# Kernel tuning notes

Hardware: AMD Instinct MI355X
Metric: run time of the kernel (lower is better)

## Reference

```python
import jax, jax.numpy as jnp
import numpy as np

N_HEAD = 12
ROPE_BASE = 10000.0


def rotate_half(x):
    h = x.shape[-1] // 2
    x1, x2 = x[..., :h], x[..., h:]
    return jnp.concatenate((-x2, x1), axis=-1)


def rope_cos_sin(T, head_dim, dtype):
    inv_freq = 1.0 / (ROPE_BASE ** (jnp.arange(0, head_dim, 2, dtype=jnp.float32) / head_dim))
    t = jnp.arange(T, dtype=jnp.float32)
    freqs = jnp.einsum('i,j->ij', t, inv_freq)          # [T, head_dim/2]
    emb = jnp.concatenate((freqs, freqs), axis=-1)       # [T, head_dim]
    return jnp.cos(emb).astype(dtype), jnp.sin(emb).astype(dtype)


def setup_inputs() -> dict:
    key = jax.random.key(0)
    ks = jax.random.split(key, 5)
    B, T, C = 1, 4096, 768
    return {
        'x': jax.random.normal(ks[0], (B, T, C), dtype=jnp.float32),
        'w_attn': jax.random.normal(ks[1], (C, 3 * C), dtype=jnp.float32) * (1.0 / np.sqrt(C)),
        'b_attn': jax.random.normal(ks[2], (3 * C,), dtype=jnp.float32) * 0.02,
        'w_proj': jax.random.normal(ks[3], (C, C), dtype=jnp.float32) * (1.0 / np.sqrt(C)),
        'b_proj': jax.random.normal(ks[4], (C,), dtype=jnp.float32) * 0.02,
    }


def reference(x, w_attn, b_attn, w_proj, b_proj):
    B, T, C = x.shape
    H = N_HEAD
    hd = C // H

    qkv = x @ w_attn + b_attn                            # [B, T, 3C]
    q, k, v = jnp.split(qkv, 3, axis=-1)
    q = q.reshape(B, T, H, hd)
    k = k.reshape(B, T, H, hd)
    v = v.reshape(B, T, H, hd)

    cos, sin = rope_cos_sin(T, hd, x.dtype)              # [T, hd]
    cos = cos[None, :, None, :]
    sin = sin[None, :, None, :]
    q = q * cos + rotate_half(q) * sin
    k = k * cos + rotate_half(k) * sin

    # [B, H, T, hd]
    q = q.transpose(0, 2, 1, 3)
    k = k.transpose(0, 2, 1, 3)
    v = v.transpose(0, 2, 1, 3)

    att = jnp.einsum('bhtd,bhsd->bhts', q, k) * (1.0 / np.sqrt(hd))
    causal_mask = jnp.triu(jnp.ones((T, T), dtype=bool), k=1)
    att = jnp.where(causal_mask, -jnp.inf, att)
    att = jax.nn.softmax(att, axis=-1)

    y = jnp.einsum('bhts,bhsd->bhtd', att, v)            # [B, H, T, hd]
    y = y.transpose(0, 2, 1, 3).reshape(B, T, C)
    return y @ w_proj + b_proj
```

## Files before the change

kernel.cpp:

```cpp
#include <hip/hip_runtime.h>
#include <hip/hip_bf16.h>
#include <math.h>

using bf16 = __hip_bfloat16;
typedef __bf16 bf16x8_t __attribute__((ext_vector_type(8)));
typedef float f32x4_t __attribute__((ext_vector_type(4)));

static __device__ __forceinline__ f32x4_t mfma16(bf16x8_t a, bf16x8_t b, f32x4_t c) {
    return __builtin_amdgcn_mfma_f32_16x16x32_bf16(a, b, c, 0, 0, 0);
}

#if __has_builtin(__builtin_amdgcn_exp2f)
#define EXP2F __builtin_amdgcn_exp2f
#else
#define EXP2F exp2f
#endif

static __device__ __forceinline__ void sincos_rev(float rev, float* s, float* c) {
    float f = rev - floorf(rev);
#if __has_builtin(__builtin_amdgcn_sinf) && __has_builtin(__builtin_amdgcn_cosf)
    *s = __builtin_amdgcn_sinf(f);
    *c = __builtin_amdgcn_cosf(f);
#else
    float th = f * 6.2831853071795864f;
    *s = __sinf(th); *c = __cosf(th);
#endif
}

static __device__ __forceinline__ void async16(bf16* lds, const bf16* g) {
    __builtin_amdgcn_global_load_lds(
        (const __attribute__((address_space(1))) unsigned int*)g,
        (__attribute__((address_space(3))) unsigned int*)lds, 16, 0, 0);
}

static __device__ __forceinline__ int detect_bf16(const unsigned short* u16) {
    const int lane = threadIdx.x & 63;
    int sane = 0;
#pragma unroll
    for (int j = 0; j < 4; ++j) {
        const unsigned short u = u16[2 * (lane * 4 + j)];
        const int e = (u >> 7) & 0xFF;
        if (u == 0 || (e >= 100 && e <= 150)) sane++;
    }
#pragma unroll
    for (int off = 1; off <= 32; off <<= 1) sane += __shfl_xor(sane, off);
    return (sane * 2 >= 256) ? 1 : 0;
}

static __device__ __forceinline__ float bias_at(const void* b, int i, int isbf) {
    return isbf ? __bfloat162float(((const bf16*)b)[i]) : ((const float*)b)[i];
}

static __device__ __forceinline__ void transpose_tile(
    const void* in, bf16* out, int in_ld, int out_ld, int bx, int by,
    int isbf, bf16 (*tile)[72]) {
    const int c0 = bx * 64, r0 = by * 64;
    const int tid = threadIdx.x;
    for (int c = tid; c < 512; c += 256) {
        const int r = c >> 3, co = (c & 7) << 3;
        if (isbf) {
            *reinterpret_cast<float4*>(&tile[r][co]) =
                *reinterpret_cast<const float4*>((const bf16*)in + (size_t)(r0 + r) * in_ld + c0 + co);
        } else {
            const float* f = (const float*)in + (size_t)(r0 + r) * in_ld + c0 + co;
            const float4 a = *reinterpret_cast<const float4*>(f);
            const float4 b = *reinterpret_cast<const float4*>(f + 4);
            tile[r][co + 0] = __float2bfloat16(a.x); tile[r][co + 1] = __float2bfloat16(a.y);
            tile[r][co + 2] = __float2bfloat16(a.z); tile[r][co + 3] = __float2bfloat16(a.w);
            tile[r][co + 4] = __float2bfloat16(b.x); tile[r][co + 5] = __float2bfloat16(b.y);
            tile[r][co + 6] = __float2bfloat16(b.z); tile[r][co + 7] = __float2bfloat16(b.w);
        }
    }
    __syncthreads();
    for (int c = tid; c < 512; c += 256) {
        const int r = c >> 3, co = (c & 7) << 3;
        union { float4 v; bf16 e[8]; } u;
#pragma unroll
        for (int j = 0; j < 8; ++j) u.e[j] = tile[co + j][r];
        *reinterpret_cast<float4*>(out + (size_t)(c0 + r) * out_ld + r0 + co) = u.v;
    }
}

__global__ __launch_bounds__(256) void prep_kernel(
    const void* __restrict__ x, const void* __restrict__ w_attn,
    const void* __restrict__ w_proj, bf16* __restrict__ xb,
    bf16* __restrict__ wAT, bf16* __restrict__ wPT) {
    __shared__ bf16 tile[64][72];
    const int isbf = detect_bf16((const unsigned short*)x);
    const int b = blockIdx.x;
    if (b < 432) {
        transpose_tile(w_attn, wAT, 2304, 768, b % 36, b / 36, isbf, tile);
    } else if (b < 576) {
        const int bb = b - 432;
        transpose_tile(w_proj, wPT, 768, 768, bb % 12, bb / 12, isbf, tile);
    } else {
        const int i = ((b - 576) * 256 + threadIdx.x) * 8;
        if (isbf) {
            *reinterpret_cast<float4*>(xb + i) =
                *reinterpret_cast<const float4*>((const bf16*)x + i);
        } else {
            const float* f = (const float*)x + i;
            const float4 a = *reinterpret_cast<const float4*>(f);
            const float4 c = *reinterpret_cast<const float4*>(f + 4);
            union { float4 v; bf16 e[8]; } u;
            u.e[0] = __float2bfloat16(a.x); u.e[1] = __float2bfloat16(a.y);
            u.e[2] = __float2bfloat16(a.z); u.e[3] = __float2bfloat16(a.w);
            u.e[4] = __float2bfloat16(c.x); u.e[5] = __float2bfloat16(c.y);
            u.e[6] = __float2bfloat16(c.z); u.e[7] = __float2bfloat16(c.w);
            *reinterpret_cast<float4*>(xb + i) = u.v;
        }
    }
}

template <int MI>
__global__ __launch_bounds__(256, MI == 4 ? 3 : 4) void gemm_kernel(
    const bf16* __restrict__ A, const bf16* __restrict__ Bt,
    const void* __restrict__ bias, bf16* __restrict__ C,
    bf16* __restrict__ VtOut, const unsigned short* __restrict__ xdet,
    int N, int K, int mode, int flexout) {
    constexpr int MT = MI * 32;
    __shared__ bf16 smem[(MT + 128) * 64];
    bf16* sa = smem;
    bf16* sb = smem + MT * 64;
    const int tid = threadIdx.x, lane = tid & 63, w = tid >> 6;
    const int wm = w >> 1, wn = w & 1, quad = lane >> 4, l16 = lane & 15;
    const int m0 = blockIdx.y * MT, n0 = blockIdx.x * 128;
    const int strow = lane >> 3, stslot = lane & 7;

    const bf16* ag[MI]; const bf16* bgp[4];
#pragma unroll
    for (int i = 0; i < MI; ++i) {
        const int r = (w * MI + i) * 8 + strow;
        ag[i] = A + (size_t)(m0 + r) * K + (stslot ^ (r & 7)) * 8;
    }
#pragma unroll
    for (int i = 0; i < 4; ++i) {
        const int r = (w * 4 + i) * 8 + strow;
        bgp[i] = Bt + (size_t)(n0 + r) * K + (stslot ^ (r & 7)) * 8;
    }

    f32x4_t acc[MI][4];
#pragma unroll
    for (int i = 0; i < MI; ++i)
#pragma unroll
        for (int j = 0; j < 4; ++j) acc[i][j] = (f32x4_t){0.f, 0.f, 0.f, 0.f};

    for (int k0 = 0; k0 < K; k0 += 64) {
        __syncthreads();
#pragma unroll
        for (int i = 0; i < MI; ++i) async16(&sa[(w * MI + i) * 512], ag[i] + k0);
#pragma unroll
        for (int i = 0; i < 4; ++i)  async16(&sb[(w * 4 + i) * 512], bgp[i] + k0);
        __asm__ __volatile__("s_waitcnt vmcnt(0)" ::: "memory");
        __syncthreads();

#pragma unroll
        for (int kk = 0; kk < 2; ++kk) {
            bf16x8_t af[MI], bf_[4];
#pragma unroll
            for (int mi = 0; mi < MI; ++mi) {
                const int r = wm * (MI * 16) + mi * 16 + l16;
                af[mi] = *reinterpret_cast<const bf16x8_t*>(
                    &sa[r * 64 + (((kk * 4 + quad) ^ (r & 7)) << 3)]);
            }
#pragma unroll
            for (int ni = 0; ni < 4; ++ni) {
                const int r = wn * 64 + ni * 16 + l16;
                bf_[ni] = *reinterpret_cast<const bf16x8_t*>(
                    &sb[r * 64 + (((kk * 4 + quad) ^ (r & 7)) << 3)]);
            }
#pragma unroll
            for (int mi = 0; mi < MI; ++mi)
#pragma unroll
                for (int ni = 0; ni < 4; ++ni)
                    acc[mi][ni] = mfma16(af[mi], bf_[ni], acc[mi][ni]);
        }
    }

    const int isbf = detect_bf16(xdet);
    const int f32out = flexout && !isbf;
    const int colbase = n0 + wn * 64;
    const int rowbase = m0 + wm * (MI * 16);
    if (mode == 1 && colbase < 1536) {
        const bool isq = colbase < 768;
        const float QS = 0.18033688011112042f;
#pragma unroll
        for (int ni = 0; ni < 2; ++ni) {
            const int d = ni * 16 + l16;
            const int col_lo = colbase + d, col_hi = col_lo + 32;
            const float blo = bias_at(bias, col_lo, isbf);
            const float bhi = bias_at(bias, col_hi, isbf);
            const float invf_rev = powf(10000.0f, -(float)d * (1.0f / 32.0f)) * 0.15915494309189535f;
#pragma unroll
            for (int mi = 0; mi < MI; ++mi) {
#pragma unroll
                for (int rg = 0; rg < 4; ++rg) {
                    const int t = rowbase + mi * 16 + quad * 4 + rg;
                    float sv, cv;
                    sincos_rev((float)t * invf_rev, &sv, &cv);
                    const float lo = acc[mi][ni][rg] + blo;
                    const float hi = acc[mi][ni + 2][rg] + bhi;
                    float nlo = lo * cv - hi * sv;
                    float nhi = hi * cv + lo * sv;
                    if (isq) { nlo *= QS; nhi *= QS; }
                    C[(size_t)t * N + col_lo] = __float2bfloat16(nlo);
                    C[(size_t)t * N + col_hi] = __float2bfloat16(nhi);
                }
            }
        }
    } else if (mode == 1) {
        if constexpr (MI == 4) {
            __syncthreads();
            bf16* T = smem + w * 2304;
            const int vcb = colbase - 1536;
#pragma unroll
            for (int pass = 0; pass < 2; ++pass) {
                if (pass) __asm__ __volatile__("s_waitcnt lgkmcnt(0)" ::: "memory");
#pragma unroll
                for (int nl = 0; nl < 2; ++nl) {
                    const int ni = pass * 2 + nl;
                    const float b = bias_at(bias, colbase + ni * 16 + l16, isbf);
                    const int dh = nl * 16 + l16;
#pragma unroll
                    for (int rg = 0; rg < 4; ++rg) {
                        union { int2 v; bf16 e[4]; } pk;
#pragma unroll
                        for (int mi = 0; mi < 4; ++mi)
                            pk.e[mi] = __float2bfloat16(acc[mi][ni][rg] + b);
                        *reinterpret_cast<int2*>(&T[dh * 72 + quad * 16 + rg * 4]) = pk.v;
                    }
                }
                __asm__ __volatile__("s_waitcnt lgkmcnt(0)" ::: "memory");
#pragma unroll
                for (int s = 0; s < 4; ++s) {
                    const int dh = s * 8 + (lane >> 3);
                    const int pj = lane & 7;
                    const float4 vv = *reinterpret_cast<const float4*>(&T[dh * 72 + pj * 8]);
                    *reinterpret_cast<float4*>(
                        &VtOut[(size_t)(vcb + pass * 32 + dh) * 4096 + rowbase + pj * 8]) = vv;
                }
            }
        }
    } else {
#pragma unroll
        for (int ni = 0; ni < 4; ++ni) {
            const int col = colbase + ni * 16 + l16;
            const float b = bias_at(bias, col, isbf);
#pragma unroll
            for (int mi = 0; mi < MI; ++mi) {
#pragma unroll
                for (int rg = 0; rg < 4; ++rg) {
                    const int t = rowbase + mi * 16 + quad * 4 + rg;
                    const float v = acc[mi][ni][rg] + b;
                    if (f32out) ((float*)C)[(size_t)t * N + col] = v;
                    else        C[(size_t)t * N + col] = __float2bfloat16(v);
                }
            }
        }
    }
}

__global__ __launch_bounds__(128, 3) void attn_kernel(
    const bf16* __restrict__ qkv, const bf16* __restrict__ Vt,
    bf16* __restrict__ ybuf, bf16* __restrict__ po, float* __restrict__ pl) {
    const int h = blockIdx.y;
    const int bx = blockIdx.x;
    int qt, c, nc;
    if (bx < 16)      { qt = bx;                 c = 0;             nc = 1; }
    else if (bx < 48) { qt = 16 + (bx - 16) / 2; c = (bx - 16) % 2; nc = 2; }
    else if (bx < 96) { qt = 32 + (bx - 48) / 3; c = (bx - 48) % 3; nc = 3; }
    else              { qt = 48 + (bx - 96) / 4; c = (bx - 96) % 4; nc = 4; }
    const int kt0 = c * 16;
    const int kt1 = min(kt0 + 16, qt + 1);

    const int tid = threadIdx.x, lane = tid & 63, w = tid >> 6;
    const int quad = lane >> 4, l16 = lane & 15, sw = l16 & 7;

    __shared__ bf16 Kt[2][4096];
    __shared__ bf16 Pt[2][2][16][72];

    const int strow = lane >> 3, stslot = lane & 7;
    const bf16* kg[4];
#pragma unroll
    for (int i = 0; i < 4; ++i) {
        const int key = (w * 4 + i) * 8 + strow;
        kg[i] = qkv + (size_t)key * 2304 + 768 + h * 64 + (stslot ^ (key & 7)) * 8;
    }
    const bf16* vbase = Vt + (size_t)(h * 64) * 4096;

    const int qbase = qt * 64 + w * 32;
    bf16x8_t qf[2][2];
#pragma unroll
    for (int f = 0; f < 2; ++f)
#pragma unroll
        for (int kc = 0; kc < 2; ++kc)
            qf[f][kc] = *reinterpret_cast<const bf16x8_t*>(
                qkv + (size_t)(qbase + f * 16 + l16) * 2304 + h * 64 + kc * 32 + quad * 8);

    f32x4_t o[2][4];
#pragma unroll
    for (int f = 0; f < 2; ++f)
#pragma unroll
        for (int dt = 0; dt < 4; ++dt) o[f][dt] = (f32x4_t){0.f, 0.f, 0.f, 0.f};
    float l_i[2][4] = {{0.f, 0.f, 0.f, 0.f}, {0.f, 0.f, 0.f, 0.f}};

#pragma unroll
    for (int i = 0; i < 4; ++i)
        async16(&Kt[0][(w * 4 + i) * 512], kg[i] + (size_t)kt0 * 64 * 2304);
    __asm__ __volatile__("s_waitcnt vmcnt(0)" ::: "memory");
    __syncthreads();

    for (int kt = kt0; kt < kt1; ++kt) {
        const int b = (kt - kt0) & 1;
        if (kt + 1 < kt1) {
#pragma unroll
            for (int i = 0; i < 4; ++i)
                async16(&Kt[b ^ 1][(w * 4 + i) * 512], kg[i] + (size_t)(kt + 1) * 64 * 2304);
        }
        bf16x8_t vf[2][4];
#pragma unroll
        for (int kc = 0; kc < 2; ++kc)
#pragma unroll
            for (int dt = 0; dt < 4; ++dt)
                vf[kc][dt] = *reinterpret_cast<const bf16x8_t*>(
                    vbase + (size_t)(dt * 16 + l16) * 4096 + kt * 64 + kc * 32 + quad * 8);

        bf16x8_t kf[2][4];
#pragma unroll
        for (int kc = 0; kc < 2; ++kc)
#pragma unroll
            for (int ct = 0; ct < 4; ++ct)
                kf[kc][ct] = *reinterpret_cast<const bf16x8_t*>(
                    &Kt[b][((ct * 16 + l16) << 6) + (((kc * 4 + quad) ^ sw) << 3)]);

        f32x4_t s[2][4];
#pragma unroll
        for (int f = 0; f < 2; ++f)
#pragma unroll
            for (int ct = 0; ct < 4; ++ct) {
                s[f][ct] = mfma16(qf[f][0], kf[0][ct], (f32x4_t){0.f, 0.f, 0.f, 0.f});
                s[f][ct] = mfma16(qf[f][1], kf[1][ct], s[f][ct]);
            }

        if (kt == qt) {
#pragma unroll
            for (int f = 0; f < 2; ++f) {
                const int rowb = qbase + f * 16 + quad * 4;
#pragma unroll
                for (int ct = 0; ct < 4; ++ct) {
                    const int key = kt * 64 + ct * 16 + l16;
#pragma unroll
                    for (int rg = 0; rg < 4; ++rg)
                        if (key > rowb + rg) s[f][ct][rg] = -INFINITY;
                }
            }
        }

#pragma unroll
        for (int f = 0; f < 2; ++f)
#pragma unroll
            for (int ct = 0; ct < 4; ++ct)
#pragma unroll
                for (int rg = 0; rg < 4; ++rg) {
                    const float p = EXP2F(s[f][ct][rg]);
                    s[f][ct][rg] = p;
                    l_i[f][rg] += p;
                }

#pragma unroll
        for (int f = 0; f < 2; ++f)
#pragma unroll
            for (int rg = 0; rg < 4; ++rg) {
                union { int2 v; __hip_bfloat162 h2[2]; } pk;
                pk.h2[0] = __float22bfloat162_rn(float2{s[f][0][rg], s[f][1][rg]});
                pk.h2[1] = __float22bfloat162_rn(float2{s[f][2][rg], s[f][3][rg]});
                *reinterpret_cast<int2*>(&Pt[w][f][quad * 4 + rg][l16 * 4]) = pk.v;
            }
        __asm__ __volatile__("s_waitcnt lgkmcnt(0)" ::: "memory");

#pragma unroll
        for (int f = 0; f < 2; ++f)
#pragma unroll
            for (int kc = 0; kc < 2; ++kc) {
                const bf16x8_t pf =
                    *reinterpret_cast<const bf16x8_t*>(&Pt[w][f][l16][kc * 32 + quad * 8]);
#pragma unroll
                for (int dt = 0; dt < 4; ++dt)
                    o[f][dt] = mfma16(pf, vf[kc][dt], o[f][dt]);
            }

        __asm__ __volatile__("s_waitcnt vmcnt(0)" ::: "memory");
        __syncthreads();
    }

#pragma unroll
    for (int off = 1; off <= 8; off <<= 1)
#pragma unroll
        for (int f = 0; f < 2; ++f)
#pragma unroll
            for (int rg = 0; rg < 4; ++rg) l_i[f][rg] += __shfl_xor(l_i[f][rg], off);

    if (nc == 1) {
#pragma unroll
        for (int f = 0; f < 2; ++f) {
            float linv[4];
#pragma unroll
            for (int rg = 0; rg < 4; ++rg)
                linv[rg] = (l_i[f][rg] > 0.f) ? 1.0f / l_i[f][rg] : 0.f;
#pragma unroll
            for (int dt = 0; dt < 4; ++dt)
#pragma unroll
                for (int rg = 0; rg < 4; ++rg)
                    ybuf[(size_t)(qbase + f * 16 + quad * 4 + rg) * 768 + h * 64 + dt * 16 + l16] =
                        __float2bfloat16(o[f][dt][rg] * linv[rg]);
        }
    } else {
#pragma unroll
        for (int f = 0; f < 2; ++f) {
            float linv[4];
#pragma unroll
            for (int rg = 0; rg < 4; ++rg)
                linv[rg] = (l_i[f][rg] > 0.f) ? 1.0f / l_i[f][rg] : 0.f;
#pragma unroll
            for (int dt = 0; dt < 4; ++dt)
#pragma unroll
                for (int rg = 0; rg < 4; ++rg) {
                    const int row = qbase + f * 16 + quad * 4 + rg;
                    po[((size_t)((h << 12) + row) * 4 + c) * 64 + dt * 16 + l16] =
                        __float2bfloat16(o[f][dt][rg] * linv[rg]);
                }
            if (l16 == 0) {
#pragma unroll
                for (int rg = 0; rg < 4; ++rg) {
                    const int row = qbase + f * 16 + quad * 4 + rg;
                    pl[((h << 12) + row) * 4 + c] = l_i[f][rg];
                }
            }
        }
    }
}

__global__ __launch_bounds__(256) void combine_kernel(
    const bf16* __restrict__ po, const float* __restrict__ pl,
    bf16* __restrict__ ybuf) {
    const int g = blockIdx.x * 256 + threadIdx.x;
    if (g >= 12 * 3072 * 64) return;
    const int d = g & 63;
    const int rr = (g >> 6) % 3072;
    const int h = g / (3072 * 64);
    const int r = 1024 + rr;
    const int nc = (r >> 6) / 16 + 1;
    const int base = ((h << 12) + r) * 4;
    float wsum = 0.f, acc = 0.f;
    for (int cc = 0; cc < nc; ++cc) {
        const float wgt = pl[base + cc];
        wsum += wgt;
        acc += wgt * __bfloat162float(po[(size_t)(base + cc) * 64 + d]);
    }
    ybuf[(size_t)r * 768 + h * 64 + d] = __float2bfloat16(acc / wsum);
}

extern "C" void kernel_launch(void* const* d_in, const int* in_sizes, int n_in,
                              void* d_out, int out_size, void* d_ws, size_t ws_size,
                              hipStream_t stream) {
    bf16* qkv  = (bf16*)d_ws;
    bf16* wAT  = qkv + (size_t)4096 * 2304;
    bf16* wPT  = wAT + (size_t)2304 * 768;
    bf16* Vt   = wPT + (size_t)768 * 768;
    bf16* ybuf = Vt + (size_t)768 * 4096;
    bf16* xb   = ybuf + (size_t)4096 * 768;
    bf16* po   = xb + (size_t)4096 * 768;
    float* pl  = (float*)(po + (size_t)12 * 4096 * 4 * 64);
    const unsigned short* xdet = (const unsigned short*)d_in[0];

    prep_kernel<<<2112, 256, 0, stream>>>(d_in[0], d_in[1], d_in[3], xb, wAT, wPT);
    gemm_kernel<4><<<dim3(18, 32), 256, 0, stream>>>(
        xb, wAT, d_in[2], qkv, Vt, xdet, 2304, 768, 1, 0);
    attn_kernel<<<dim3(160, 12), 128, 0, stream>>>(qkv, Vt, ybuf, po, pl);
    combine_kernel<<<9216, 256, 0, stream>>>(po, pl, ybuf);
    gemm_kernel<1><<<dim3(6, 128), 256, 0, stream>>>(
        ybuf, wPT, d_in[4], (bf16*)d_out, nullptr, xdet, 768, 768, 0, 1);
}
```

Baseline: 203.9 us.

## Stage V tiles through swizzled LDS with single-buffered K/V async prefetch

```diff
diff --git a/kernel.cpp b/kernel.cpp
--- a/kernel.cpp
+++ b/kernel.cpp
@@ -276,17 +276,20 @@
     const int tid = threadIdx.x, lane = tid & 63, w = tid >> 6;
     const int quad = lane >> 4, l16 = lane & 15, sw = l16 & 7;
 
-    __shared__ bf16 Kt[2][4096];
+    __shared__ bf16 Kt[4096];
+    __shared__ bf16 Vs[4096];
     __shared__ bf16 Pt[2][2][16][72];
 
     const int strow = lane >> 3, stslot = lane & 7;
-    const bf16* kg[4];
+    const bf16* kg[4]; const bf16* vg[4];
 #pragma unroll
     for (int i = 0; i < 4; ++i) {
-        const int key = (w * 4 + i) * 8 + strow;
+        const int ch = w * 4 + i;
+        const int key = ch * 8 + strow;
         kg[i] = qkv + (size_t)key * 2304 + 768 + h * 64 + (stslot ^ (key & 7)) * 8;
-    }
-    const bf16* vbase = Vt + (size_t)(h * 64) * 4096;
+        const int d = ch * 8 + strow;
+        vg[i] = Vt + (size_t)(h * 64 + d) * 4096 + (stslot ^ (d & 7)) * 8;
+    }
 
     const int qbase = qt * 64 + w * 32;
     bf16x8_t qf[2][2];
@@ -305,33 +308,36 @@
     float l_i[2][4] = {{0.f, 0.f, 0.f, 0.f}, {0.f, 0.f, 0.f, 0.f}};
 
 #pragma unroll
-    for (int i = 0; i < 4; ++i)
-        async16(&Kt[0][(w * 4 + i) * 512], kg[i] + (size_t)kt0 * 64 * 2304);
+    for (int i = 0; i < 4; ++i) {
+        async16(&Kt[(w * 4 + i) * 512], kg[i] + (size_t)kt0 * 64 * 2304);
+        async16(&Vs[(w * 4 + i) * 512], vg[i] + (size_t)kt0 * 64);
+    }
     __asm__ __volatile__("s_waitcnt vmcnt(0)" ::: "memory");
     __syncthreads();
 
     for (int kt = kt0; kt < kt1; ++kt) {
-        const int b = (kt - kt0) & 1;
-        if (kt + 1 < kt1) {
-#pragma unroll
-            for (int i = 0; i < 4; ++i)
-                async16(&Kt[b ^ 1][(w * 4 + i) * 512], kg[i] + (size_t)(kt + 1) * 64 * 2304);
-        }
-        bf16x8_t vf[2][4];
+        bf16x8_t kf[2][4], vf[2][4];
+#pragma unroll
+        for (int kc = 0; kc < 2; ++kc)
+#pragma unroll
+            for (int ct = 0; ct < 4; ++ct)
+                kf[kc][ct] = *reinterpret_cast<const bf16x8_t*>(
+                    &Kt[((ct * 16 + l16) << 6) + (((kc * 4 + quad) ^ sw) << 3)]);
 #pragma unroll
         for (int kc = 0; kc < 2; ++kc)
 #pragma unroll
             for (int dt = 0; dt < 4; ++dt)
                 vf[kc][dt] = *reinterpret_cast<const bf16x8_t*>(
-                    vbase + (size_t)(dt * 16 + l16) * 4096 + kt * 64 + kc * 32 + quad * 8);
-
-        bf16x8_t kf[2][4];
-#pragma unroll
-        for (int kc = 0; kc < 2; ++kc)
-#pragma unroll
-            for (int ct = 0; ct < 4; ++ct)
-                kf[kc][ct] = *reinterpret_cast<const bf16x8_t*>(
-                    &Kt[b][((ct * 16 + l16) << 6) + (((kc * 4 + quad) ^ sw) << 3)]);
+                    &Vs[((dt * 16 + l16) << 6) + (((kc * 4 + quad) ^ sw) << 3)]);
+        __syncthreads();
+
+        if (kt + 1 < kt1) {
+#pragma unroll
+            for (int i = 0; i < 4; ++i) {
+                async16(&Kt[(w * 4 + i) * 512], kg[i] + (size_t)(kt + 1) * 64 * 2304);
+                async16(&Vs[(w * 4 + i) * 512], vg[i] + (size_t)(kt + 1) * 64);
+            }
+        }
 
         f32x4_t s[2][4];
 #pragma unroll
```

Result: faster. 181.2 us (-11.1%).
